# Kernel tuning notes

Hardware: AMD Instinct MI355X
Metric: run time of the kernel (lower is better)

The kernel has to match this reference:

```python
import jax, jax.numpy as jnp
import numpy as np

B, T, C = 4, 2048, 1024
H = 16
HD = C // H  # 64
OBS_DIM, ACT_DIM = 17, 6
JOINED_DIM = OBS_DIM + ACT_DIM + 2  # 25


def _make_mask():
    # tril causal mask with every (JOINED_DIM-1 + k*JOINED_DIM)-th column zeroed (RL branch)
    m = np.tril(np.ones((T, T), dtype=np.float32))
    m[:, JOINED_DIM - 1::JOINED_DIM] = 0.0
    return jnp.asarray(m > 0)  # bool [T, T]


MASK = _make_mask()


def setup_inputs() -> dict:
    key = jax.random.key(0)
    ks = jax.random.split(key, 9)
    s = 1.0 / np.sqrt(C)
    return {
        "x": jax.random.normal(ks[0], (B, T, C), dtype=jnp.float32),
        "Wq": jax.random.normal(ks[1], (C, C), dtype=jnp.float32) * s,
        "bq": jax.random.normal(ks[2], (C,), dtype=jnp.float32) * s,
        "Wk": jax.random.normal(ks[3], (C, C), dtype=jnp.float32) * s,
        "bk": jax.random.normal(ks[4], (C,), dtype=jnp.float32) * s,
        "Wv": jax.random.normal(ks[5], (C, C), dtype=jnp.float32) * s,
        "bv": jax.random.normal(ks[6], (C,), dtype=jnp.float32) * s,
        "Wp": jax.random.normal(ks[7], (C, C), dtype=jnp.float32) * s,
        "bp": jax.random.normal(ks[8], (C,), dtype=jnp.float32) * s,
    }


def reference(x, Wq, bq, Wk, bk, Wv, bv, Wp, bp):
    # torch nn.Linear: y = x @ W.T + b
    def split_heads(t):  # [B,T,C] -> [B,H,T,HD]
        return t.reshape(B, T, H, HD).transpose(0, 2, 1, 3)

    q = split_heads(x @ Wq.T + bq)
    k = split_heads(x @ Wk.T + bk)
    v = split_heads(x @ Wv.T + bv)

    att = jnp.einsum("bhqd,bhkd->bhqk", q, k) * (1.0 / np.sqrt(HD))
    att = jnp.where(MASK[None, None, :, :], att, -jnp.inf)
    att = jax.nn.softmax(att, axis=-1)
    # dropout layers are identity in eval mode

    y = jnp.einsum("bhqk,bhkd->bhqd", att, v)  # [B,H,T,HD]
    y = y.transpose(0, 2, 1, 3).reshape(B, T, C)
    return y @ Wp.T + bp
```

## Files before the change

### kernel.cpp

```cpp
#include <hip/hip_runtime.h>
#include <hip/hip_bf16.h>


typedef __attribute__((ext_vector_type(8))) short short8;
typedef __attribute__((ext_vector_type(4))) float floatx4;
typedef unsigned short us;

__device__ __forceinline__ us f2bf(float f){
    union { __hip_bfloat16 h; us u; } cv;
    cv.h = __float2bfloat16(f);
    return cv.u;
}

__device__ __forceinline__ void ld_g2l16(const void* g, void* l){
    __builtin_amdgcn_global_load_lds((const __attribute__((address_space(1))) void*)g,
                                     (__attribute__((address_space(3))) void*)l, 16, 0, 0);
}

__global__ __launch_bounds__(256) void cvt_kernel(const float* __restrict__ in,
                                                  us* __restrict__ out, int n4){
    int i = blockIdx.x * 256 + threadIdx.x;
    if (i < n4){
        float4 v = reinterpret_cast<const float4*>(in)[i];
        ushort4 o;
        o.x = f2bf(v.x); o.y = f2bf(v.y); o.z = f2bf(v.z); o.w = f2bf(v.w);
        reinterpret_cast<ushort4*>(out)[i] = o;
    }
}

__global__ __launch_bounds__(256) void cvt4_kernel(const float* __restrict__ w0, const float* __restrict__ w1,
                                                   const float* __restrict__ w2, const float* __restrict__ w3,
                                                   us* __restrict__ o0, us* __restrict__ o1,
                                                   us* __restrict__ o2, us* __restrict__ o3){
    int wsel = blockIdx.x >> 10;
    int i = (blockIdx.x & 1023) * 256 + threadIdx.x;
    const float* src = (wsel == 0) ? w0 : (wsel == 1) ? w1 : (wsel == 2) ? w2 : w3;
    us* dst = (wsel == 0) ? o0 : (wsel == 1) ? o1 : (wsel == 2) ? o2 : o3;
    float4 v = reinterpret_cast<const float4*>(src)[i];
    ushort4 o;
    o.x = f2bf(v.x); o.y = f2bf(v.y); o.z = f2bf(v.z); o.w = f2bf(v.w);
    reinterpret_cast<ushort4*>(dst)[i] = o;
}

#define QSCALE 0.1803368801111244f
__global__ __launch_bounds__(256) void gemm_qkv(
    const us* __restrict__ A,
    const us* __restrict__ Wqb, const us* __restrict__ Wkb, const us* __restrict__ Wvb,
    const float* __restrict__ bq, const float* __restrict__ bk, const float* __restrict__ bv,
    us* __restrict__ qo, us* __restrict__ ko, us* __restrict__ vto)
{
    __shared__ us smem[128*64*2];
    us* lA = smem;
    us* lB = smem + 128*64;
    const int tid = threadIdx.x;
    const int lane = tid & 63;
    const int wave = tid >> 6;
    const int lane15 = lane & 15;
    const int quad = lane >> 4;
    const int wm = wave >> 1, wn = wave & 1;
    const int seg = blockIdx.x >> 3;
    const int n_loc = (blockIdx.x & 7) * 128;
    const int m0 = blockIdx.y * 128;

    const us* Wb = (seg == 0) ? Wqb : (seg == 1) ? Wkb : Wvb;
    const float* bias = (seg == 0) ? bq : (seg == 1) ? bk : bv;

    floatx4 zero = {0.f, 0.f, 0.f, 0.f};
    floatx4 acc[4][4];
    #pragma unroll
    for (int i = 0; i < 4; i++)
        #pragma unroll
        for (int j = 0; j < 4; j++) acc[i][j] = zero;

    int srow[4], sg[4];
    #pragma unroll
    for (int t = 0; t < 4; t++){
        int s = (t*4 + wave)*64 + lane;
        srow[t] = s >> 3;
        sg[t] = (s & 7) ^ ((s >> 3) & 7);
    }

    for (int k0 = 0; k0 < 1024; k0 += 64){
        #pragma unroll
        for (int t = 0; t < 4; t++){
            int chunk = t*4 + wave;
            ld_g2l16(A  + (size_t)(m0 + srow[t])*1024 + k0 + sg[t]*8, &lA[chunk*512]);
            ld_g2l16(Wb + (size_t)(n_loc + srow[t])*1024 + k0 + sg[t]*8, &lB[chunk*512]);
        }
        __syncthreads();
        #pragma unroll
        for (int ks = 0; ks < 2; ks++){
            short8 af[4], bf[4];
            #pragma unroll
            for (int i = 0; i < 4; i++){
                int ra = wm*64 + i*16 + lane15;
                int ga = (ks*4 + quad) ^ (ra & 7);
                af[i] = *reinterpret_cast<const short8*>(&lA[ra*64 + ga*8]);
                int rb = wn*64 + i*16 + lane15;
                int gb = (ks*4 + quad) ^ (rb & 7);
                bf[i] = *reinterpret_cast<const short8*>(&lB[rb*64 + gb*8]);
            }
            #pragma unroll
            for (int i = 0; i < 4; i++)
                #pragma unroll
                for (int j = 0; j < 4; j++)
                    acc[i][j] = __builtin_amdgcn_mfma_f32_16x16x32_bf16(af[i], bf[j], acc[i][j], 0, 0, 0);
        }
        __syncthreads();
    }

    if (seg < 2){
        #pragma unroll
        for (int i = 0; i < 4; i++){
            #pragma unroll
            for (int j = 0; j < 4; j++){
                int n = n_loc + wn*64 + j*16 + lane15;
                float bvv = bias[n];
                #pragma unroll
                for (int r = 0; r < 4; r++){
                    int m = m0 + wm*64 + i*16 + quad*4 + r;
                    float val = acc[i][j][r] + bvv;
                    if (seg == 0){
                        qo[(size_t)m*1024 + n] = f2bf(val * QSCALE);
                    } else {
                        int b = m >> 11, t = m & 2047;
                        int h = n >> 6,  d = n & 63;
                        ko[(((size_t)b*16 + h)*2048 + t)*64 + d] = f2bf(val);
                    }
                }
            }
        }
    } else {
        us* lCT = smem;
        const int b = m0 >> 11;
        const int t0 = m0 & 2047;
        #pragma unroll
        for (int p = 0; p < 2; p++){
            if (p) __syncthreads();
            if (wm == p){
                #pragma unroll
                for (int j = 0; j < 4; j++){
                    int nl = wn*64 + j*16 + lane15;
                    float bvv = bias[n_loc + nl];
                    #pragma unroll
                    for (int i = 0; i < 4; i++){
                        int ml = i*16 + quad*4;
                        unsigned int lo = (unsigned int)f2bf(acc[i][j][0] + bvv) |
                                          ((unsigned int)f2bf(acc[i][j][1] + bvv) << 16);
                        unsigned int hi = (unsigned int)f2bf(acc[i][j][2] + bvv) |
                                          ((unsigned int)f2bf(acc[i][j][3] + bvv) << 16);
                        uint2 pk2; pk2.x = lo; pk2.y = hi;
                        *reinterpret_cast<uint2*>(&lCT[nl*68 + ml]) = pk2;
                    }
                }
            }
            __syncthreads();
            int np = tid >> 1;
            int half = tid & 1;
            int nC = n_loc + np;
            int h = nC >> 6, d = nC & 63;
            us* dst = vto + (((size_t)b*16 + h)*64 + d)*2048 + t0 + p*64 + half*32;
            #pragma unroll
            for (int i = 0; i < 4; i++){
                uint4 v = *reinterpret_cast<const uint4*>(&lCT[np*68 + half*32 + i*8]);
                *reinterpret_cast<uint4*>(dst + i*8) = v;
            }
        }
    }
}

__device__ __forceinline__ void pstore_rg(
    floatx4 (&s)[4], us* pw, bool diag, int rgrow, int j0, int jr, const int (&res)[4],
    int lane15, int quad)
{
    #pragma unroll
    for (int tj = 0; tj < 4; tj++){
        bool bad = (res[tj] + jr) == 24;
        #pragma unroll
        for (int r = 0; r < 4; r++){
            float p = __builtin_amdgcn_exp2f(s[tj][r]);
            bool kill = bad || (diag && (j0 + tj*16 + lane15 > rgrow + quad*4 + r));
            pw[(quad*4 + r)*72 + tj*16 + lane15] = f2bf(kill ? 0.f : p);
        }
    }
}

__global__ __launch_bounds__(256, 3) void flash_attn(
    const us* __restrict__ q,
    const us* __restrict__ k,
    const us* __restrict__ vT,
    us* __restrict__ y)
{
    __shared__ us lK[2][64*64];
    __shared__ us lV[2][64*64];
    __shared__ us lP[4][2][16*72];
    const int tid = threadIdx.x;
    const int lane = tid & 63;
    const int wave = tid >> 6;
    const int lane15 = lane & 15;
    const int quad = lane >> 4;
    const int lin = blockIdx.x;
    const int qt2 = 15 - (lin >> 6);
    const int bh = lin & 63;
    const int b = bh >> 4, h = bh & 15;
    const int rg0 = qt2*128 + wave*16;
    const int rg1 = rg0 + 64;
    const int nIter = 2*qt2 + 2;

    const us* kb = k  + (size_t)bh*2048*64;
    const us* vb = vT + (size_t)bh*64*2048;

    const us* q0 = q + ((size_t)b*2048 + rg0 + lane15)*1024 + h*64 + quad*8;
    const us* q1 = q + ((size_t)b*2048 + rg1 + lane15)*1024 + h*64 + quad*8;
    short8 qf0a = *reinterpret_cast<const short8*>(q0);
    short8 qf0b = *reinterpret_cast<const short8*>(q0 + 32);
    short8 qf1a = *reinterpret_cast<const short8*>(q1);
    short8 qf1b = *reinterpret_cast<const short8*>(q1 + 32);

    floatx4 zero = {0.f, 0.f, 0.f, 0.f};
    floatx4 acc0[4], acc1[4];
    #pragma unroll
    for (int d = 0; d < 4; d++){ acc0[d] = zero; acc1[d] = zero; }
    floatx4 lacc0 = zero, lacc1 = zero;

    us* pw0 = &lP[wave][0][0];
    us* pw1 = &lP[wave][1][0];

    short8 onesb;
    #pragma unroll
    for (int e = 0; e < 8; e++) onesb[e] = (short)0x3F80;

    int res[4];
    #pragma unroll
    for (int tj = 0; tj < 4; tj++) res[tj] = (tj*16 + lane15) % 25;
    int jr = 0;

    int srow[2], sgr[2];
    #pragma unroll
    for (int i = 0; i < 2; i++){
        int s = (i*4 + wave)*64 + lane;
        srow[i] = s >> 3;
        sgr[i] = (s & 7) ^ ((s >> 3) & 7);
    }

    #pragma unroll
    for (int i = 0; i < 2; i++){
        ld_g2l16(kb + (size_t)srow[i]*64 + sgr[i]*8, &lK[0][(i*4 + wave)*512]);
        ld_g2l16(vb + (size_t)srow[i]*2048 + sgr[i]*8, &lV[0][(i*4 + wave)*512]);
    }

    for (int it = 0; it < nIter; it++){
        const int j0 = it*64;
        __syncthreads();

        if (it + 1 < nIter){
            #pragma unroll
            for (int i = 0; i < 2; i++){
                ld_g2l16(kb + (size_t)(j0 + 64 + srow[i])*64 + sgr[i]*8,
                         &lK[(it + 1) & 1][(i*4 + wave)*512]);
                ld_g2l16(vb + (size_t)srow[i]*2048 + j0 + 64 + sgr[i]*8,
                         &lV[(it + 1) & 1][(i*4 + wave)*512]);
            }
        }

        const us* Kb = lK[it & 1];
        const us* Vb = lV[it & 1];
        const bool act0  = (it + 1 < nIter);
        const bool diag0 = (it + 2 == nIter);
        const bool diag1 = (it + 1 == nIter);

        floatx4 s0[4], s1[4];
        #pragma unroll
        for (int tj = 0; tj < 4; tj++){
            int rk = tj*16 + lane15;
            short8 kf0 = *reinterpret_cast<const short8*>(&Kb[rk*64 + ((quad     ^ (rk & 7)))*8]);
            short8 kf1 = *reinterpret_cast<const short8*>(&Kb[rk*64 + (((4+quad) ^ (rk & 7)))*8]);
            floatx4 z1 = __builtin_amdgcn_mfma_f32_16x16x32_bf16(qf1a, kf0, zero, 0, 0, 0);
            s1[tj]     = __builtin_amdgcn_mfma_f32_16x16x32_bf16(qf1b, kf1, z1,   0, 0, 0);
            if (act0){
                floatx4 z0 = __builtin_amdgcn_mfma_f32_16x16x32_bf16(qf0a, kf0, zero, 0, 0, 0);
                s0[tj]     = __builtin_amdgcn_mfma_f32_16x16x32_bf16(qf0b, kf1, z0,   0, 0, 0);
            }
        }

        pstore_rg(s1, pw1, diag1, rg1, j0, jr, res, lane15, quad);
        if (act0)
            pstore_rg(s0, pw0, diag0, rg0, j0, jr, res, lane15, quad);

        #pragma unroll
        for (int ks = 0; ks < 2; ks++){
            short8 pf1 = *reinterpret_cast<const short8*>(&pw1[lane15*72 + ks*32 + quad*8]);
            short8 pf0 = *reinterpret_cast<const short8*>(&pw0[lane15*72 + ks*32 + quad*8]);
            lacc1 = __builtin_amdgcn_mfma_f32_16x16x32_bf16(pf1, onesb, lacc1, 0, 0, 0);
            if (act0) lacc0 = __builtin_amdgcn_mfma_f32_16x16x32_bf16(pf0, onesb, lacc0, 0, 0, 0);
            #pragma unroll
            for (int dt = 0; dt < 4; dt++){
                int rv = dt*16 + lane15;
                short8 vf = *reinterpret_cast<const short8*>(&Vb[rv*64 + (((ks*4+quad) ^ (rv & 7)))*8]);
                acc1[dt] = __builtin_amdgcn_mfma_f32_16x16x32_bf16(pf1, vf, acc1[dt], 0, 0, 0);
                if (act0) acc0[dt] = __builtin_amdgcn_mfma_f32_16x16x32_bf16(pf0, vf, acc0[dt], 0, 0, 0);
            }
        }

        jr += 14; if (jr >= 25) jr -= 25;
    }

    float rl0[4], rl1[4];
    #pragma unroll
    for (int r = 0; r < 4; r++){ rl0[r] = 1.0f / lacc0[r]; rl1[r] = 1.0f / lacc1[r]; }
    #pragma unroll
    for (int dt = 0; dt < 4; dt++){
        #pragma unroll
        for (int r = 0; r < 4; r++){
            int t0 = rg0 + quad*4 + r;
            int t1 = rg1 + quad*4 + r;
            int cc = h*64 + dt*16 + lane15;
            y[((size_t)b*2048 + t0)*1024 + cc] = f2bf(acc0[dt][r] * rl0[r]);
            y[((size_t)b*2048 + t1)*1024 + cc] = f2bf(acc1[dt][r] * rl1[r]);
        }
    }
}

__global__ __launch_bounds__(256) void gemm_out(
    const us* __restrict__ A,
    const us* __restrict__ Wb,
    const float* __restrict__ bias,
    float* __restrict__ out)
{
    __shared__ us lA[128*64];
    __shared__ us lB[128*64];
    const int tid = threadIdx.x;
    const int lane = tid & 63;
    const int wave = tid >> 6;
    const int lane15 = lane & 15;
    const int quad = lane >> 4;
    const int wm = wave >> 1, wn = wave & 1;
    const int m0 = blockIdx.y * 128;
    const int n0 = blockIdx.x * 128;

    floatx4 zero = {0.f, 0.f, 0.f, 0.f};
    floatx4 acc[4][4];
    #pragma unroll
    for (int i = 0; i < 4; i++)
        #pragma unroll
        for (int j = 0; j < 4; j++) acc[i][j] = zero;

    int srow[4], sg[4];
    #pragma unroll
    for (int t = 0; t < 4; t++){
        int s = (t*4 + wave)*64 + lane;
        srow[t] = s >> 3;
        sg[t] = (s & 7) ^ ((s >> 3) & 7);
    }

    for (int k0 = 0; k0 < 1024; k0 += 64){
        #pragma unroll
        for (int t = 0; t < 4; t++){
            int chunk = t*4 + wave;
            ld_g2l16(A  + (size_t)(m0 + srow[t])*1024 + k0 + sg[t]*8, &lA[chunk*512]);
            ld_g2l16(Wb + (size_t)(n0 + srow[t])*1024 + k0 + sg[t]*8, &lB[chunk*512]);
        }
        __syncthreads();
        #pragma unroll
        for (int ks = 0; ks < 2; ks++){
            short8 af[4], bf[4];
            #pragma unroll
            for (int i = 0; i < 4; i++){
                int ra = wm*64 + i*16 + lane15;
                int ga = (ks*4 + quad) ^ (ra & 7);
                af[i] = *reinterpret_cast<const short8*>(&lA[ra*64 + ga*8]);
                int rb = wn*64 + i*16 + lane15;
                int gb = (ks*4 + quad) ^ (rb & 7);
                bf[i] = *reinterpret_cast<const short8*>(&lB[rb*64 + gb*8]);
            }
            #pragma unroll
            for (int i = 0; i < 4; i++)
                #pragma unroll
                for (int j = 0; j < 4; j++)
                    acc[i][j] = __builtin_amdgcn_mfma_f32_16x16x32_bf16(af[i], bf[j], acc[i][j], 0, 0, 0);
        }
        __syncthreads();
    }

    #pragma unroll
    for (int i = 0; i < 4; i++){
        #pragma unroll
        for (int j = 0; j < 4; j++){
            int n = n0 + wn*64 + j*16 + lane15;
            float bvv = bias[n];
            #pragma unroll
            for (int r = 0; r < 4; r++){
                int m = m0 + wm*64 + i*16 + quad*4 + r;
                out[(size_t)m*1024 + n] = acc[i][j][r] + bvv;
            }
        }
    }
}

extern "C" void kernel_launch(void* const* d_in, const int* in_sizes, int n_in,
                              void* d_out, int out_size, void* d_ws, size_t ws_size,
                              hipStream_t stream)
{
    const float* x  = (const float*)d_in[0];
    const float* Wq = (const float*)d_in[1];
    const float* bq = (const float*)d_in[2];
    const float* Wk = (const float*)d_in[3];
    const float* bk = (const float*)d_in[4];
    const float* Wv = (const float*)d_in[5];
    const float* bv = (const float*)d_in[6];
    const float* Wp = (const float*)d_in[7];
    const float* bp = (const float*)d_in[8];
    float* out = (float*)d_out;

    us* ws  = (us*)d_ws;
    us* xbf = ws;
    us* wqb = xbf + (size_t)8192*1024;
    us* wkb = wqb + (size_t)1024*1024;
    us* wvb = wkb + (size_t)1024*1024;
    us* wpb = wvb + (size_t)1024*1024;
    us* qws = wpb + (size_t)1024*1024;
    us* kws = qws + (size_t)8388608;
    us* vtw = kws + (size_t)8388608;
    us* yws = vtw + (size_t)8388608;

    cvt_kernel<<<8192, 256, 0, stream>>>(x, xbf, 2097152);
    cvt4_kernel<<<4096, 256, 0, stream>>>(Wq, Wk, Wv, Wp, wqb, wkb, wvb, wpb);

    gemm_qkv<<<dim3(24, 64), 256, 0, stream>>>(xbf, wqb, wkb, wvb, bq, bk, bv, qws, kws, vtw);

    flash_attn<<<1024, 256, 0, stream>>>(qws, kws, vtw, yws);

    gemm_out<<<dim3(8, 64), 256, 0, stream>>>(yws, wpb, bp, out);
}
```

Baseline: 269.0 us.

## Rewrite QKV GEMM as 256x256-tile, 8-wave, double-buffered pipelined kernel

Replaces the 128x128 single-buffered QKV projection GEMM with a 256x256 tile kernel using 512 threads and 128 KB of double-buffered LDS. It stages global-to-LDS loads for the next k-tile in quarter slices, interleaved with MFMA quadrants under explicit barriers, vmcnt/lgkmcnt waits and setprio. This is meant to hide memory latency and raise data reuse per tile. The costs are fewer blocks (384), heavy register and LDS pressure, and a fragile hand-written wait schedule.

Result: no change. 266.3 us (-1.0%).

```diff
diff --git a/kernel.cpp b/kernel.cpp
--- a/kernel.cpp
+++ b/kernel.cpp
@@ -42,90 +42,167 @@
     reinterpret_cast<ushort4*>(dst)[i] = o;
 }
 
+
 #define QSCALE 0.1803368801111244f
-__global__ __launch_bounds__(256) void gemm_qkv(
+
+#define BAR() __builtin_amdgcn_s_barrier()
+#define LGKM0() do { asm volatile("s_waitcnt lgkmcnt(0)" ::: "memory"); __builtin_amdgcn_sched_barrier(0); } while(0)
+#define VMC2() asm volatile("s_waitcnt vmcnt(2)" ::: "memory")
+#define VMC0() asm volatile("s_waitcnt vmcnt(0)" ::: "memory")
+
+#define STAGE_A8(buf, half, kt) do { \
+    _Pragma("unroll") \
+    for (int i_ = 0; i_ < 2; i_++) \
+        ld_g2l16(A + (size_t)(m0 + (half)*128 + srow[i_])*1024 + (kt)*64 + sgr[i_]*8, \
+                 &smem[(buf)*16384 + (half)*8192 + (i_*8 + wave)*512]); \
+} while(0)
+
+#define STAGE_B8(buf, half, kt) do { \
+    _Pragma("unroll") \
+    for (int i_ = 0; i_ < 2; i_++) \
+        ld_g2l16(Wb + (size_t)(n0 + (half)*128 + srow[i_])*1024 + (kt)*64 + sgr[i_]*8, \
+                 &smem[32768 + (buf)*16384 + (half)*8192 + (i_*8 + wave)*512]); \
+} while(0)
+
+#define LOAD_AF8(buf, IH) do { \
+    _Pragma("unroll") \
+    for (int i_ = 0; i_ < 4; i_++){ \
+        int ra_ = wm*128 + (IH)*64 + i_*16 + lane15; \
+        _Pragma("unroll") \
+        for (int ks_ = 0; ks_ < 2; ks_++){ \
+            int ga_ = (ks_*4 + quad) ^ (ra_ & 7); \
+            af[i_][ks_] = *reinterpret_cast<const short8*>(&smem[(buf)*16384 + ra_*64 + ga_*8]); \
+        } } \
+} while(0)
+
+#define LOAD_BF8(buf, JH) do { \
+    _Pragma("unroll") \
+    for (int j_ = 0; j_ < 2; j_++){ \
+        int rb_ = wn*64 + (JH)*32 + j_*16 + lane15; \
+        _Pragma("unroll") \
+        for (int ks_ = 0; ks_ < 2; ks_++){ \
+            int gb_ = (ks_*4 + quad) ^ (rb_ & 7); \
+            bf[JH][j_][ks_] = *reinterpret_cast<const short8*>(&smem[32768 + (buf)*16384 + rb_*64 + gb_*8]); \
+        } } \
+} while(0)
+
+#define MFMA_Q8(IH, JH) do { \
+    __builtin_amdgcn_s_setprio(1); \
+    _Pragma("unroll") \
+    for (int ks_ = 0; ks_ < 2; ks_++) \
+        _Pragma("unroll") \
+        for (int i_ = 0; i_ < 4; i_++) \
+            _Pragma("unroll") \
+            for (int j_ = 0; j_ < 2; j_++) \
+                acc[(IH)*4 + i_][(JH)*2 + j_] = __builtin_amdgcn_mfma_f32_16x16x32_bf16( \
+                    af[i_][ks_], bf[JH][j_][ks_], acc[(IH)*4 + i_][(JH)*2 + j_], 0, 0, 0); \
+    __builtin_amdgcn_s_setprio(0); \
+} while(0)
+
+__global__ __launch_bounds__(512, 2) void gemm_qkv8(
     const us* __restrict__ A,
     const us* __restrict__ Wqb, const us* __restrict__ Wkb, const us* __restrict__ Wvb,
     const float* __restrict__ bq, const float* __restrict__ bk, const float* __restrict__ bv,
     us* __restrict__ qo, us* __restrict__ ko, us* __restrict__ vto)
 {
-    __shared__ us smem[128*64*2];
-    us* lA = smem;
-    us* lB = smem + 128*64;
+    __shared__ us smem[65536];
     const int tid = threadIdx.x;
     const int lane = tid & 63;
     const int wave = tid >> 6;
     const int lane15 = lane & 15;
     const int quad = lane >> 4;
-    const int wm = wave >> 1, wn = wave & 1;
-    const int seg = blockIdx.x >> 3;
-    const int n_loc = (blockIdx.x & 7) * 128;
-    const int m0 = blockIdx.y * 128;
+    const int wm = wave >> 2;
+    const int wn = wave & 3;
+    const int seg = blockIdx.x >> 2;
+    const int n0 = (blockIdx.x & 3) * 256;
+    const int m0 = blockIdx.y * 256;
 
     const us* Wb = (seg == 0) ? Wqb : (seg == 1) ? Wkb : Wvb;
     const float* bias = (seg == 0) ? bq : (seg == 1) ? bk : bv;
 
+    int srow[2], sgr[2];
+    #pragma unroll
+    for (int i = 0; i < 2; i++){
+        int s = (i*8 + wave)*64 + lane;
+        srow[i] = s >> 3;
+        sgr[i] = (s & 7) ^ ((s >> 3) & 7);
+    }
+
     floatx4 zero = {0.f, 0.f, 0.f, 0.f};
-    floatx4 acc[4][4];
-    #pragma unroll
-    for (int i = 0; i < 4; i++)
+    floatx4 acc[8][4];
+    #pragma unroll
+    for (int i = 0; i < 8; i++)
         #pragma unroll
         for (int j = 0; j < 4; j++) acc[i][j] = zero;
-
-    int srow[4], sg[4];
-    #pragma unroll
-    for (int t = 0; t < 4; t++){
-        int s = (t*4 + wave)*64 + lane;
-        srow[t] = s >> 3;
-        sg[t] = (s & 7) ^ ((s >> 3) & 7);
-    }
-
-    for (int k0 = 0; k0 < 1024; k0 += 64){
-        #pragma unroll
-        for (int t = 0; t < 4; t++){
-            int chunk = t*4 + wave;
-            ld_g2l16(A  + (size_t)(m0 + srow[t])*1024 + k0 + sg[t]*8, &lA[chunk*512]);
-            ld_g2l16(Wb + (size_t)(n_loc + srow[t])*1024 + k0 + sg[t]*8, &lB[chunk*512]);
-        }
-        __syncthreads();
-        #pragma unroll
-        for (int ks = 0; ks < 2; ks++){
-            short8 af[4], bf[4];
-            #pragma unroll
-            for (int i = 0; i < 4; i++){
-                int ra = wm*64 + i*16 + lane15;
-                int ga = (ks*4 + quad) ^ (ra & 7);
-                af[i] = *reinterpret_cast<const short8*>(&lA[ra*64 + ga*8]);
-                int rb = wn*64 + i*16 + lane15;
-                int gb = (ks*4 + quad) ^ (rb & 7);
-                bf[i] = *reinterpret_cast<const short8*>(&lB[rb*64 + gb*8]);
-            }
-            #pragma unroll
-            for (int i = 0; i < 4; i++)
-                #pragma unroll
-                for (int j = 0; j < 4; j++)
-                    acc[i][j] = __builtin_amdgcn_mfma_f32_16x16x32_bf16(af[i], bf[j], acc[i][j], 0, 0, 0);
-        }
-        __syncthreads();
+    short8 af[4][2];
+    short8 bf[2][2][2];
+
+    STAGE_A8(0, 0, 0); STAGE_A8(0, 1, 0); STAGE_B8(0, 0, 0); STAGE_B8(0, 1, 0);
+    STAGE_A8(1, 0, 1);
+    VMC2(); BAR();
+
+    #pragma unroll 1
+    for (int it = 0; it < 8; it++){
+        const int t = 2*it;
+        LOAD_AF8(0, 0); LOAD_BF8(0, 0);
+        STAGE_A8(1, 1, t+1);
+        BAR(); LGKM0();
+        MFMA_Q8(0, 0);
+        BAR();
+        LOAD_BF8(0, 1);
+        STAGE_B8(1, 0, t+1);
+        BAR(); LGKM0();
+        MFMA_Q8(0, 1);
+        BAR();
+        LOAD_AF8(0, 1);
+        STAGE_B8(1, 1, t+1);
+        BAR(); LGKM0();
+        MFMA_Q8(1, 1);
+        BAR();
+        if (it < 7) STAGE_A8(0, 0, t+2);
+        BAR(); LGKM0();
+        MFMA_Q8(1, 0);
+        if (it < 7) { VMC2(); } else { VMC0(); }
+        BAR();
+        LOAD_AF8(1, 0); LOAD_BF8(1, 0);
+        if (it < 7) STAGE_A8(0, 1, t+2);
+        BAR(); LGKM0();
+        MFMA_Q8(0, 0);
+        BAR();
+        LOAD_BF8(1, 1);
+        if (it < 7) STAGE_B8(0, 0, t+2);
+        BAR(); LGKM0();
+        MFMA_Q8(0, 1);
+        BAR();
+        LOAD_AF8(1, 1);
+        if (it < 7) STAGE_B8(0, 1, t+2);
+        BAR(); LGKM0();
+        MFMA_Q8(1, 1);
+        BAR();
+        if (it < 7) STAGE_A8(1, 0, t+3);
+        BAR(); LGKM0();
+        MFMA_Q8(1, 0);
+        if (it < 7) { VMC2(); } else { VMC0(); }
+        BAR();
     }
 
     if (seg < 2){
         #pragma unroll
-        for (int i = 0; i < 4; i++){
+        for (int i = 0; i < 8; i++){
             #pragma unroll
             for (int j = 0; j < 4; j++){
-                int n = n_loc + wn*64 + j*16 + lane15;
+                int n = n0 + wn*64 + j*16 + lane15;
                 float bvv = bias[n];
                 #pragma unroll
                 for (int r = 0; r < 4; r++){
-                    int m = m0 + wm*64 + i*16 + quad*4 + r;
+                    int m = m0 + wm*128 + i*16 + quad*4 + r;
                     float val = acc[i][j][r] + bvv;
                     if (seg == 0){
                         qo[(size_t)m*1024 + n] = f2bf(val * QSCALE);
                     } else {
-                        int b = m >> 11, t = m & 2047;
+                        int b = m >> 11, tt = m & 2047;
                         int h = n >> 6,  d = n & 63;
-                        ko[(((size_t)b*16 + h)*2048 + t)*64 + d] = f2bf(val);
+                        ko[(((size_t)b*16 + h)*2048 + tt)*64 + d] = f2bf(val);
                     }
                 }
             }
@@ -141,29 +218,29 @@
                 #pragma unroll
                 for (int j = 0; j < 4; j++){
                     int nl = wn*64 + j*16 + lane15;
-                    float bvv = bias[n_loc + nl];
+                    float bvv = bias[n0 + nl];
                     #pragma unroll
-                    for (int i = 0; i < 4; i++){
+                    for (int i = 0; i < 8; i++){
                         int ml = i*16 + quad*4;
                         unsigned int lo = (unsigned int)f2bf(acc[i][j][0] + bvv) |
                                           ((unsigned int)f2bf(acc[i][j][1] + bvv) << 16);
                         unsigned int hi = (unsigned int)f2bf(acc[i][j][2] + bvv) |
                                           ((unsigned int)f2bf(acc[i][j][3] + bvv) << 16);
                         uint2 pk2; pk2.x = lo; pk2.y = hi;
-                        *reinterpret_cast<uint2*>(&lCT[nl*68 + ml]) = pk2;
+                        *reinterpret_cast<uint2*>(&lCT[(size_t)nl*136 + ml]) = pk2;
                     }
                 }
             }
             __syncthreads();
-            int np = tid >> 1;
+            int nl = tid >> 1;
             int half = tid & 1;
-            int nC = n_loc + np;
+            int nC = n0 + nl;
             int h = nC >> 6, d = nC & 63;
-            us* dst = vto + (((size_t)b*16 + h)*64 + d)*2048 + t0 + p*64 + half*32;
-            #pragma unroll
-            for (int i = 0; i < 4; i++){
-                uint4 v = *reinterpret_cast<const uint4*>(&lCT[np*68 + half*32 + i*8]);
-                *reinterpret_cast<uint4*>(dst + i*8) = v;
+            us* dst = vto + (((size_t)b*16 + h)*64 + d)*2048 + t0 + p*128 + half*64;
+            #pragma unroll
+            for (int ii = 0; ii < 8; ii++){
+                uint4 v = *reinterpret_cast<const uint4*>(&lCT[(size_t)nl*136 + half*64 + ii*8]);
+                *reinterpret_cast<uint4*>(dst + ii*8) = v;
             }
         }
     }
@@ -426,7 +503,7 @@
     cvt_kernel<<<8192, 256, 0, stream>>>(x, xbf, 2097152);
     cvt4_kernel<<<4096, 256, 0, stream>>>(Wq, Wk, Wv, Wp, wqb, wkb, wvb, wpb);
 
-    gemm_qkv<<<dim3(24, 64), 256, 0, stream>>>(xbf, wqb, wkb, wvb, bq, bk, bv, qws, kws, vtw);
+    gemm_qkv8<<<dim3(12, 32), 512, 0, stream>>>(xbf, wqb, wkb, wvb, bq, bk, bv, qws, kws, vtw);
 
     flash_attn<<<1024, 256, 0, stream>>>(qws, kws, vtw, yws);
 
```
